# Kernel tuning notes

Hardware: AMD Instinct MI355X
Metric: run time of the kernel (lower is better)

Reference implementation:

```python
import jax, jax.numpy as jnp
import numpy as np

EMBED_DIM = 1024
N_HEADS = 16
HEAD_DIM = EMBED_DIM // N_HEADS
N_CATS = 5
SCALE = float(np.sqrt(HEAD_DIM))


def setup_inputs() -> dict:
    key = jax.random.key(0)
    ks = jax.random.split(key, 16)
    B, S = 2, 2048
    inp = {
        "query": jax.random.normal(ks[0], (B, S, EMBED_DIM), jnp.float32),
        "key_": jax.random.normal(ks[1], (B, S, EMBED_DIM), jnp.float32),
        "value": jax.random.normal(ks[2], (B, S, EMBED_DIM), jnp.float32),
        "responses": jax.random.randint(ks[3], (B, S), 0, N_CATS),
        "mask": jnp.ones((B, S, S), jnp.int32),
        # Linear params (torch convention: y = x @ W.T + b)
        "Wq": jax.random.normal(ks[4], (EMBED_DIM, EMBED_DIM), jnp.float32) * 0.02,
        "bq": jnp.zeros((EMBED_DIM,), jnp.float32),
        "Wk": jax.random.normal(ks[5], (EMBED_DIM, EMBED_DIM), jnp.float32) * 0.02,
        "bk": jnp.zeros((EMBED_DIM,), jnp.float32),
        "Wv": jax.random.normal(ks[6], (EMBED_DIM, EMBED_DIM), jnp.float32) * 0.02,
        "bv": jnp.zeros((EMBED_DIM,), jnp.float32),
        "Wo": jax.random.normal(ks[7], (EMBED_DIM, EMBED_DIM), jnp.float32) * 0.02,
        "bo": jnp.zeros((EMBED_DIM,), jnp.float32),
        # qwk_modulation: Linear(1, n_heads)
        "Wm": jax.random.normal(ks[8], (N_HEADS, 1), jnp.float32) * 0.5,
        "bm": jnp.zeros((N_HEADS,), jnp.float32),
    }
    return inp


def _qwk_matrix():
    i = jnp.arange(N_CATS, dtype=jnp.float32)
    return 1.0 - (i[:, None] - i[None, :]) ** 2 / (N_CATS - 1) ** 2  # [C, C]


def reference(query, key_, value, responses, mask,
              Wq, bq, Wk, bk, Wv, bv, Wo, bo, Wm, bm):
    B, S, E = query.shape
    # projections
    Q = (query @ Wq.T + bq).reshape(B, S, N_HEADS, HEAD_DIM).transpose(0, 2, 1, 3)
    K = (key_ @ Wk.T + bk).reshape(B, S, N_HEADS, HEAD_DIM).transpose(0, 2, 1, 3)
    V = (value @ Wv.T + bv).reshape(B, S, N_HEADS, HEAD_DIM).transpose(0, 2, 1, 3)
    scores = jnp.einsum("bhqd,bhkd->bhqk", Q, K) / SCALE  # [B,H,S,S]
    # QWK ordinal bias: gather pairwise weight, tiny linear 1->H, broadcast-add
    qwk = _qwk_matrix()
    pair = qwk[responses[:, :, None], responses[:, None, :]]  # [B,S,S]
    # Linear(1, n_heads): bias[...,None] @ Wm.T + bm -> [B,S,S,H] -> [B,H,S,S]
    head_bias = pair[:, None, :, :] * Wm[:, 0][None, :, None, None] + bm[None, :, None, None]
    scores = scores + head_bias
    scores = jnp.where(mask[:, None, :, :] == 0, -1e9, scores)
    attn = jax.nn.softmax(scores, axis=-1)
    attended = jnp.einsum("bhqk,bhkd->bhqd", attn, V)
    attended = attended.transpose(0, 2, 1, 3).reshape(B, S, E)
    return attended @ Wo.T + bo
```

## Files before the change

### kernel.cpp

```cpp
#include <hip/hip_runtime.h>
#include <hip/hip_bf16.h>
#include <stdint.h>

#define S_LEN 2048
#define EMB   1024
#define NHEAD 16
#define HDIM  64
#define BATCH 2

typedef __bf16 bf16x8 __attribute__((ext_vector_type(8)));
typedef float  f32x4  __attribute__((ext_vector_type(4)));

__device__ __forceinline__ void gll16(const void* g, void* l) {
  __builtin_amdgcn_global_load_lds(
      (const __attribute__((address_space(1))) void*)g,
      (__attribute__((address_space(3))) void*)l,
      16, 0, 0);
}

__global__ void __launch_bounds__(256) cast_mask_kernel(
    const float* __restrict__ s0, const float* __restrict__ s1, const float* __restrict__ s2,
    const float* __restrict__ s3, const float* __restrict__ s4, const float* __restrict__ s5,
    const float* __restrict__ s6,
    __hip_bfloat16* __restrict__ d0, __hip_bfloat16* __restrict__ d1,
    __hip_bfloat16* __restrict__ d2, __hip_bfloat16* __restrict__ d3,
    __hip_bfloat16* __restrict__ d4, __hip_bfloat16* __restrict__ d5,
    __hip_bfloat16* __restrict__ d6,
    const int* __restrict__ mask, unsigned* __restrict__ flags) {
  const int z = blockIdx.y;
  const int t = threadIdx.x;
  if (z == 7) {
    const int kt = blockIdx.x & 15, qt = (blockIdx.x >> 4) & 31, b = (int)blockIdx.x >> 9;
    const int* base = mask + ((size_t)b * S_LEN + (size_t)qt * 64) * S_LEN + (size_t)kt * 128;
    int ok = 1;
#pragma unroll
    for (int p = 0; p < 8; ++p) {
      int idx = p * 256 + t;
      int row = idx >> 5, c4 = idx & 31;
      const int4 v = *(const int4*)(base + (size_t)row * S_LEN + c4 * 4);
      ok &= (v.x != 0) & (v.y != 0) & (v.z != 0) & (v.w != 0);
    }
    unsigned long long bl = __ballot(ok);
    __shared__ unsigned long long bw[4];
    bw[t >> 6] = bl;
    __syncthreads();
    if (t == 0) {
      unsigned all = ((bw[0] & bw[1] & bw[2] & bw[3]) == ~0ull) ? 1u : 0u;
      flags[((size_t)b * 32 + qt) * 16 + kt] = all;
    }
    return;
  }
  const float* s = (z == 0) ? s0 : (z == 1) ? s1 : (z == 2) ? s2 : (z == 3) ? s3
                 : (z == 4) ? s4 : (z == 5) ? s5 : s6;
  __hip_bfloat16* d = (z == 0) ? d0 : (z == 1) ? d1 : (z == 2) ? d2 : (z == 3) ? d3
                    : (z == 4) ? d4 : (z == 5) ? d5 : d6;
  const int n = (z < 3) ? (BATCH * S_LEN * EMB) : (EMB * EMB);
  const size_t i = ((size_t)blockIdx.x * 256 + t) * 16;
  if (i >= (size_t)n) return;
  __hip_bfloat16 tmp[16];
#pragma unroll
  for (int j = 0; j < 4; ++j) {
    const float4 v = *(const float4*)(s + i + j * 4);
    tmp[j * 4 + 0] = __float2bfloat16(v.x);
    tmp[j * 4 + 1] = __float2bfloat16(v.y);
    tmp[j * 4 + 2] = __float2bfloat16(v.z);
    tmp[j * 4 + 3] = __float2bfloat16(v.w);
  }
  *(bf16x8*)(d + i)     = *(bf16x8*)&tmp[0];
  *(bf16x8*)(d + i + 8) = *(bf16x8*)&tmp[8];
}

__global__ void __launch_bounds__(256, 2)
gemm_kernel(const __hip_bfloat16* __restrict__ A0, const __hip_bfloat16* __restrict__ A1,
            const __hip_bfloat16* __restrict__ A2,
            const __hip_bfloat16* __restrict__ W0, const __hip_bfloat16* __restrict__ W1,
            const __hip_bfloat16* __restrict__ W2,
            const float* __restrict__ b0, const float* __restrict__ b1,
            const float* __restrict__ b2,
            __hip_bfloat16* __restrict__ O0, __hip_bfloat16* __restrict__ O1,
            __hip_bfloat16* __restrict__ O2) {
  __shared__ __align__(16) __hip_bfloat16 As[128 * 64];
  __shared__ __align__(16) __hip_bfloat16 Bs[128 * 64];

  const int L = blockIdx.x;
  const int m0 = (L & 31) * 128;
  const int n0 = ((L >> 5) & 7) * 128;
  const int z  = L >> 8;

  const __hip_bfloat16* A  = (z == 0) ? A0 : ((z == 1) ? A1 : A2);
  const __hip_bfloat16* W  = (z == 0) ? W0 : ((z == 1) ? W1 : W2);
  const float* bi          = (z == 0) ? b0 : ((z == 1) ? b1 : b2);
  __hip_bfloat16* O        = (z == 0) ? O0 : ((z == 1) ? O1 : O2);

  const int t = threadIdx.x;
  const int w = t >> 6, lane = t & 63, quad = lane >> 4, l15 = lane & 15;
  const int wr = w >> 1, wc = w & 1;

  f32x4 acc[4][4];
#pragma unroll
  for (int i = 0; i < 4; ++i)
#pragma unroll
    for (int j = 0; j < 4; ++j) acc[i][j] = (f32x4)0.0f;

  const int srow = t >> 3;
  const int scb  = (t & 7) ^ (srow & 7);
  const __hip_bfloat16* Ap = A + (size_t)(m0 + srow) * EMB + (scb << 3);
  const __hip_bfloat16* Wp = W + (size_t)(n0 + srow) * EMB + (scb << 3);

  for (int k0 = 0; k0 < EMB; k0 += 64) {
    __syncthreads();
#pragma unroll
    for (int rnd = 0; rnd < 4; ++rnd) {
      gll16(Ap + (size_t)(rnd * 32) * EMB + k0, &As[(rnd * 256 + (w << 6)) * 8]);
      gll16(Wp + (size_t)(rnd * 32) * EMB + k0, &Bs[(rnd * 256 + (w << 6)) * 8]);
    }
    __syncthreads();

    bf16x8 af[4][2], bfr[4][2];
#pragma unroll
    for (int i = 0; i < 4; ++i) {
      const int ra = wr * 64 + i * 16 + l15;
#pragma unroll
      for (int hh = 0; hh < 2; ++hh)
        af[i][hh] = *(const bf16x8*)&As[ra * 64 + ((((hh << 2) + quad) ^ (l15 & 7)) << 3)];
    }
#pragma unroll
    for (int j = 0; j < 4; ++j) {
      const int rbw = wc * 64 + j * 16 + l15;
#pragma unroll
      for (int hh = 0; hh < 2; ++hh)
        bfr[j][hh] = *(const bf16x8*)&Bs[rbw * 64 + ((((hh << 2) + quad) ^ (l15 & 7)) << 3)];
    }
#pragma unroll
    for (int hh = 0; hh < 2; ++hh)
#pragma unroll
      for (int i = 0; i < 4; ++i)
#pragma unroll
        for (int j = 0; j < 4; ++j)
          acc[i][j] =
              __builtin_amdgcn_mfma_f32_16x16x32_bf16(af[i][hh], bfr[j][hh], acc[i][j], 0, 0, 0);
  }

#pragma unroll
  for (int j = 0; j < 4; ++j) {
    const int ng = n0 + wc * 64 + j * 16 + l15;
    const float bb = bi[ng];
    const int h = ng >> 6, d = ng & 63;
#pragma unroll
    for (int i = 0; i < 4; ++i) {
#pragma unroll
      for (int r = 0; r < 4; ++r) {
        const int mg = m0 + wr * 64 + i * 16 + quad * 4 + r;
        const int b = mg >> 11, s = mg & 2047;
        float v = acc[i][j][r] + bb;
        if (z == 0) {
          O[(((size_t)b * NHEAD + h) * S_LEN + s) * HDIM + d] =
              __float2bfloat16(v * (0.125f * 1.4426950408889634f));
        } else if (z == 1) {
          O[(((size_t)b * NHEAD + h) * S_LEN + s) * HDIM + d] = __float2bfloat16(v);
        } else {
          const size_t idx = (size_t)(b * NHEAD + h) * 131072 + (size_t)(s >> 7) * 8192 +
                             (size_t)((((s >> 5) & 3) * 4 + ((s >> 2) & 3)) * 64 + d) * 8 +
                             ((s >> 4) & 1) * 4 + (s & 3);
          O[idx] = __float2bfloat16(v);
        }
      }
    }
  }
}

__global__ void __launch_bounds__(256, 2)
gemm_o_kernel(const __hip_bfloat16* __restrict__ A, const __hip_bfloat16* __restrict__ W,
              const float* __restrict__ bi, float* __restrict__ O) {
  __shared__ __align__(16) __hip_bfloat16 As[64 * 64];
  __shared__ __align__(16) __hip_bfloat16 Bs[128 * 64];
  const int L = blockIdx.x;
  const int m0 = (L & 63) * 64;
  const int n0 = (L >> 6) * 128;
  const int t = threadIdx.x;
  const int w = t >> 6, lane = t & 63, quad = lane >> 4, l15 = lane & 15;
  const int wr = w >> 1, wc = w & 1;

  f32x4 acc[2][4];
#pragma unroll
  for (int i = 0; i < 2; ++i)
#pragma unroll
    for (int j = 0; j < 4; ++j) acc[i][j] = (f32x4)0.0f;

  const int srow = t >> 3;
  const int scb  = (t & 7) ^ (srow & 7);
  const __hip_bfloat16* Ap = A + (size_t)(m0 + srow) * EMB + (scb << 3);
  const __hip_bfloat16* Wp = W + (size_t)(n0 + srow) * EMB + (scb << 3);

  for (int k0 = 0; k0 < EMB; k0 += 64) {
    __syncthreads();
#pragma unroll
    for (int rnd = 0; rnd < 2; ++rnd)
      gll16(Ap + (size_t)(rnd * 32) * EMB + k0, &As[(rnd * 256 + (w << 6)) * 8]);
#pragma unroll
    for (int rnd = 0; rnd < 4; ++rnd)
      gll16(Wp + (size_t)(rnd * 32) * EMB + k0, &Bs[(rnd * 256 + (w << 6)) * 8]);
    __syncthreads();

    bf16x8 af[2][2], bfr[4][2];
#pragma unroll
    for (int i = 0; i < 2; ++i) {
      const int ra = wr * 32 + i * 16 + l15;
#pragma unroll
      for (int hh = 0; hh < 2; ++hh)
        af[i][hh] = *(const bf16x8*)&As[ra * 64 + ((((hh << 2) + quad) ^ (l15 & 7)) << 3)];
    }
#pragma unroll
    for (int j = 0; j < 4; ++j) {
      const int rbw = wc * 64 + j * 16 + l15;
#pragma unroll
      for (int hh = 0; hh < 2; ++hh)
        bfr[j][hh] = *(const bf16x8*)&Bs[rbw * 64 + ((((hh << 2) + quad) ^ (l15 & 7)) << 3)];
    }
#pragma unroll
    for (int hh = 0; hh < 2; ++hh)
#pragma unroll
      for (int i = 0; i < 2; ++i)
#pragma unroll
        for (int j = 0; j < 4; ++j)
          acc[i][j] =
              __builtin_amdgcn_mfma_f32_16x16x32_bf16(af[i][hh], bfr[j][hh], acc[i][j], 0, 0, 0);
  }

#pragma unroll
  for (int j = 0; j < 4; ++j) {
    const int ng = n0 + wc * 64 + j * 16 + l15;
    const float bb = bi[ng];
#pragma unroll
    for (int i = 0; i < 2; ++i) {
#pragma unroll
      for (int r = 0; r < 4; ++r) {
        const int mg = m0 + wr * 32 + i * 16 + quad * 4 + r;
        O[(size_t)mg * EMB + ng] = acc[i][j][r] + bb;
      }
    }
  }
}

__global__ void __launch_bounds__(512, 4)
flash_kernel(const __hip_bfloat16* __restrict__ qws, const __hip_bfloat16* __restrict__ kws,
             const __hip_bfloat16* __restrict__ vpk, const int* __restrict__ responses,
             const int* __restrict__ mask, const float* __restrict__ Wm,
             const unsigned* __restrict__ flags, __hip_bfloat16* __restrict__ att) {
  __shared__ __align__(16) unsigned char smem[32768];
  __shared__ unsigned char rb[S_LEN];
  __shared__ float lsm[512];

  __hip_bfloat16* Ks = (__hip_bfloat16*)smem;
  __hip_bfloat16* Vs = (__hip_bfloat16*)(smem + 16384);
  float* sm = (float*)smem;

  const int t = threadIdx.x;
  const int w = t >> 6, lane = t & 63, quad = lane >> 4, l15 = lane & 15;
  const int L = blockIdx.x;
  const int bh = L & 31;
  const int qt = L >> 5;
  const int b = bh >> 4, h = bh & 15;
  const int q0 = qt * 128;
  const int wq = w & 3, khalf = w >> 2;

#pragma unroll
  for (int i = 0; i < 4; ++i)
    rb[i * 512 + t] = (unsigned char)responses[b * S_LEN + i * 512 + t];

  const __hip_bfloat16* qbase = qws + ((size_t)bh * S_LEN + q0 + wq * 32) * HDIM;
  bf16x8 qf[2][2];
#pragma unroll
  for (int qg = 0; qg < 2; ++qg)
#pragma unroll
    for (int ks = 0; ks < 2; ++ks)
      qf[qg][ks] =
          *(const bf16x8*)(qbase + (size_t)(qg * 16 + l15) * HDIM + ks * 32 + quad * 8);

  const float c = Wm[h] * (0.0625f * 1.4426950408889634f);
  float A2[2];
#pragma unroll
  for (int qg = 0; qg < 2; ++qg)
    A2[qg] = 2.0f * c * (float)responses[b * S_LEN + q0 + wq * 32 + qg * 16 + l15];

  const __hip_bfloat16* kptr = kws + ((size_t)bh * S_LEN + (t >> 3)) * HDIM +
                               (((t & 7) ^ ((t >> 3) & 7)) << 3);
  const __hip_bfloat16* vptr = vpk + (size_t)bh * 131072 + (size_t)t * 8;

  float lsum[2] = {0.f, 0.f};
  f32x4 acc_o[2][4];
#pragma unroll
  for (int qg = 0; qg < 2; ++qg)
#pragma unroll
    for (int dt = 0; dt < 4; ++dt) acc_o[qg][dt] = (f32x4)0.0f;

  for (int kt = 0; kt < S_LEN / 128; ++kt) {
    __syncthreads();
#pragma unroll
    for (int p = 0; p < 2; ++p) {
      gll16(kptr + p * 64 * HDIM, &Ks[(p * 512 + (w << 6)) * 8]);
      gll16(vptr + p * 4096,      &Vs[(p * 512 + (w << 6)) * 8]);
    }
    kptr += 128 * HDIM;
    vptr += 8192;
    __syncthreads();

    const unsigned fl = flags[((size_t)b * 32 + 2 * qt + (wq >> 1)) * 16 + kt];

    bf16x8 pfr[2][2];
#pragma unroll
    for (int ct = 0; ct < 4; ++ct) {
      const int rowk = khalf * 64 + ct * 16 + l15;
      bf16x8 kf0 = *(const bf16x8*)&Ks[rowk * 64 + ((quad ^ (l15 & 7)) << 3)];
      bf16x8 kf1 = *(const bf16x8*)&Ks[rowk * 64 + (((4 + quad) ^ (l15 & 7)) << 3)];
      const unsigned ru = *(const unsigned*)&rb[kt * 128 + khalf * 64 + ct * 16 + quad * 4];
#pragma unroll
      for (int qg = 0; qg < 2; ++qg) {
        f32x4 sc = __builtin_amdgcn_mfma_f32_16x16x32_bf16(kf0, qf[qg][0], (f32x4)0.0f, 0, 0, 0);
        sc = __builtin_amdgcn_mfma_f32_16x16x32_bf16(kf1, qf[qg][1], sc, 0, 0, 0);
        __hip_bfloat16 pb[4];
#pragma unroll
        for (int r = 0; r < 4; ++r) {
          const float rkf = (float)((ru >> (8 * r)) & 255u);
          const float sb = fmaf(rkf, fmaf(-c, rkf, A2[qg]), sc[r]);
          float p = __builtin_amdgcn_exp2f(sb);
          if (!fl) {
            int mq = mask[((size_t)b * S_LEN + q0 + wq * 32 + qg * 16 + l15) * S_LEN +
                          kt * 128 + khalf * 64 + ct * 16 + quad * 4 + r];
            p = mq ? p : 0.0f;
          }
          lsum[qg] += p;
          pb[r] = __float2bfloat16(p);
        }
        __hip_bfloat16* half = (__hip_bfloat16*)&pfr[qg][ct >> 1] + (ct & 1) * 4;
        half[0] = pb[0]; half[1] = pb[1]; half[2] = pb[2]; half[3] = pb[3];
      }
    }

#pragma unroll
    for (int ct2 = 0; ct2 < 2; ++ct2) {
      const int g2 = khalf * 2 + ct2;
#pragma unroll
      for (int dt = 0; dt < 4; ++dt) {
        bf16x8 vv = *(const bf16x8*)&Vs[(((g2 << 2) + quad) * 64 + (dt << 4) + l15) << 3];
#pragma unroll
        for (int qg = 0; qg < 2; ++qg)
          acc_o[qg][dt] =
              __builtin_amdgcn_mfma_f32_16x16x32_bf16(pfr[qg][ct2], vv, acc_o[qg][dt], 0, 0, 0);
      }
    }
  }

  __syncthreads();
  if (khalf == 0) {
#pragma unroll
    for (int qg = 0; qg < 2; ++qg) {
#pragma unroll
      for (int dt = 0; dt < 4; ++dt)
        *(f32x4*)&sm[((((wq << 1) + qg) << 2) + dt) * 256 + lane * 4] = acc_o[qg][dt];
      lsm[((wq << 1) + qg) * 64 + lane] = lsum[qg];
    }
  }
  __syncthreads();
  if (khalf == 1) {
#pragma unroll
    for (int qg = 0; qg < 2; ++qg) {
      lsum[qg] += lsm[((wq << 1) + qg) * 64 + lane];
      lsum[qg] += __shfl_xor(lsum[qg], 16, 64);
      lsum[qg] += __shfl_xor(lsum[qg], 32, 64);
#pragma unroll
      for (int dt = 0; dt < 4; ++dt)
        acc_o[qg][dt] += *(const f32x4*)&sm[((((wq << 1) + qg) << 2) + dt) * 256 + lane * 4];
      float inv[4];
#pragma unroll
      for (int r = 0; r < 4; ++r) inv[r] = 1.0f / __shfl(lsum[qg], quad * 4 + r, 64);
#pragma unroll
      for (int dt = 0; dt < 4; ++dt)
#pragma unroll
        for (int r = 0; r < 4; ++r)
          att[((size_t)b * S_LEN + q0 + wq * 32 + qg * 16 + quad * 4 + r) * EMB +
              h * HDIM + dt * 16 + l15] = __float2bfloat16(acc_o[qg][dt][r] * inv[r]);
    }
  }
}

extern "C" void kernel_launch(void* const* d_in, const int* in_sizes, int n_in,
                              void* d_out, int out_size, void* d_ws, size_t ws_size,
                              hipStream_t stream) {
  const float* query = (const float*)d_in[0];
  const float* key_  = (const float*)d_in[1];
  const float* value = (const float*)d_in[2];
  const int* responses = (const int*)d_in[3];
  const int* mask      = (const int*)d_in[4];
  const float* Wq = (const float*)d_in[5];
  const float* bq = (const float*)d_in[6];
  const float* Wk = (const float*)d_in[7];
  const float* bk = (const float*)d_in[8];
  const float* Wv = (const float*)d_in[9];
  const float* bv = (const float*)d_in[10];
  const float* Wo = (const float*)d_in[11];
  const float* bo = (const float*)d_in[12];
  const float* Wm = (const float*)d_in[13];

  __hip_bfloat16* ws = (__hip_bfloat16*)d_ws;
  const size_t NTOK = (size_t)BATCH * S_LEN * EMB;
  const size_t NW   = (size_t)EMB * EMB;
  __hip_bfloat16* qcast = ws;
  __hip_bfloat16* kcast = ws + NTOK;
  __hip_bfloat16* vcast = ws + 2 * NTOK;
  __hip_bfloat16* wqb   = ws + 3 * NTOK;
  __hip_bfloat16* wkb   = wqb + NW;
  __hip_bfloat16* wvb   = wqb + 2 * NW;
  __hip_bfloat16* wob   = wqb + 3 * NW;
  __hip_bfloat16* qws   = wqb + 4 * NW;
  __hip_bfloat16* kws   = qws + NTOK;
  __hip_bfloat16* vpk   = qws + 2 * NTOK;
  __hip_bfloat16* att   = qws + 3 * NTOK;
  unsigned* flags       = (unsigned*)(qws + 4 * NTOK);
  float* out            = (float*)d_out;

  cast_mask_kernel<<<dim3(1024, 8), 256, 0, stream>>>(
      query, key_, value, Wq, Wk, Wv, Wo,
      qcast, kcast, vcast, wqb, wkb, wvb, wob, mask, flags);
  gemm_kernel<<<768, 256, 0, stream>>>(qcast, kcast, vcast, wqb, wkb, wvb,
                                       bq, bk, bv, qws, kws, vpk);
  flash_kernel<<<512, 512, 0, stream>>>(qws, kws, vpk, responses, mask,
                                        Wm, flags, att);
  gemm_o_kernel<<<512, 256, 0, stream>>>(att, wob, bo, out);
}
```

Measured before the change: 249.0 us.

## Double-buffer K/V tiles in flash kernel and prefetch mask flags

Result: slower. 254.0 us (+2.0%).

```diff
diff --git a/kernel.cpp b/kernel.cpp
--- a/kernel.cpp
+++ b/kernel.cpp
@@ -247,12 +247,10 @@
              const __hip_bfloat16* __restrict__ vpk, const int* __restrict__ responses,
              const int* __restrict__ mask, const float* __restrict__ Wm,
              const unsigned* __restrict__ flags, __hip_bfloat16* __restrict__ att) {
-  __shared__ __align__(16) unsigned char smem[32768];
+  __shared__ __align__(16) unsigned char smem[65536];
   __shared__ unsigned char rb[S_LEN];
   __shared__ float lsm[512];
 
-  __hip_bfloat16* Ks = (__hip_bfloat16*)smem;
-  __hip_bfloat16* Vs = (__hip_bfloat16*)(smem + 16384);
   float* sm = (float*)smem;
 
   const int t = threadIdx.x;
@@ -283,6 +281,13 @@
   for (int qg = 0; qg < 2; ++qg)
     A2[qg] = 2.0f * c * (float)responses[b * S_LEN + q0 + wq * 32 + qg * 16 + l15];
 
+  unsigned fmask;
+  {
+    const unsigned fv =
+        flags[((size_t)b * 32 + 2 * qt + (wq >> 1)) * 16 + (lane & 15)];
+    fmask = (unsigned)__ballot(fv != 0u);
+  }
+
   const __hip_bfloat16* kptr = kws + ((size_t)bh * S_LEN + (t >> 3)) * HDIM +
                                (((t & 7) ^ ((t >> 3) & 7)) << 3);
   const __hip_bfloat16* vptr = vpk + (size_t)bh * 131072 + (size_t)t * 8;
@@ -294,18 +299,38 @@
 #pragma unroll
     for (int dt = 0; dt < 4; ++dt) acc_o[qg][dt] = (f32x4)0.0f;
 
-  for (int kt = 0; kt < S_LEN / 128; ++kt) {
-    __syncthreads();
+  {
+    __hip_bfloat16* Kd = (__hip_bfloat16*)smem;
+    __hip_bfloat16* Vd = Kd + 8192;
 #pragma unroll
     for (int p = 0; p < 2; ++p) {
-      gll16(kptr + p * 64 * HDIM, &Ks[(p * 512 + (w << 6)) * 8]);
-      gll16(vptr + p * 4096,      &Vs[(p * 512 + (w << 6)) * 8]);
+      gll16(kptr + p * 64 * HDIM, &Kd[(p * 512 + (w << 6)) * 8]);
+      gll16(vptr + p * 4096,      &Vd[(p * 512 + (w << 6)) * 8]);
     }
     kptr += 128 * HDIM;
     vptr += 8192;
-    __syncthreads();
-
-    const unsigned fl = flags[((size_t)b * 32 + 2 * qt + (wq >> 1)) * 16 + kt];
+  }
+  asm volatile("s_waitcnt vmcnt(0) lgkmcnt(0)" ::: "memory");
+  __builtin_amdgcn_s_barrier();
+  __builtin_amdgcn_sched_barrier(0);
+
+  int cur = 0;
+  for (int kt = 0; kt < S_LEN / 128; ++kt) {
+    if (kt < S_LEN / 128 - 1) {
+      __hip_bfloat16* Kd = (__hip_bfloat16*)(smem + (cur ? 0 : 32768));
+      __hip_bfloat16* Vd = Kd + 8192;
+#pragma unroll
+      for (int p = 0; p < 2; ++p) {
+        gll16(kptr + p * 64 * HDIM, &Kd[(p * 512 + (w << 6)) * 8]);
+        gll16(vptr + p * 4096,      &Vd[(p * 512 + (w << 6)) * 8]);
+      }
+      kptr += 128 * HDIM;
+      vptr += 8192;
+    }
+    const __hip_bfloat16* Ks = (const __hip_bfloat16*)(smem + (cur ? 32768 : 0));
+    const __hip_bfloat16* Vs = Ks + 8192;
+
+    const bool fl = (fmask >> kt) & 1u;
 
     bf16x8 pfr[2][2];
 #pragma unroll
@@ -316,8 +341,10 @@
       const unsigned ru = *(const unsigned*)&rb[kt * 128 + khalf * 64 + ct * 16 + quad * 4];
 #pragma unroll
       for (int qg = 0; qg < 2; ++qg) {
+        __builtin_amdgcn_s_setprio(1);
         f32x4 sc = __builtin_amdgcn_mfma_f32_16x16x32_bf16(kf0, qf[qg][0], (f32x4)0.0f, 0, 0, 0);
         sc = __builtin_amdgcn_mfma_f32_16x16x32_bf16(kf1, qf[qg][1], sc, 0, 0, 0);
+        __builtin_amdgcn_s_setprio(0);
         __hip_bfloat16 pb[4];
 #pragma unroll
         for (int r = 0; r < 4; ++r) {
@@ -343,15 +370,21 @@
 #pragma unroll
       for (int dt = 0; dt < 4; ++dt) {
         bf16x8 vv = *(const bf16x8*)&Vs[(((g2 << 2) + quad) * 64 + (dt << 4) + l15) << 3];
+        __builtin_amdgcn_s_setprio(1);
 #pragma unroll
         for (int qg = 0; qg < 2; ++qg)
           acc_o[qg][dt] =
               __builtin_amdgcn_mfma_f32_16x16x32_bf16(pfr[qg][ct2], vv, acc_o[qg][dt], 0, 0, 0);
+        __builtin_amdgcn_s_setprio(0);
       }
     }
-  }
-
-  __syncthreads();
+
+    asm volatile("s_waitcnt vmcnt(0)" ::: "memory");
+    __builtin_amdgcn_s_barrier();
+    __builtin_amdgcn_sched_barrier(0);
+    cur ^= 1;
+  }
+
   if (khalf == 0) {
 #pragma unroll
     for (int qg = 0; qg < 2; ++qg) {
```

## Halve flash query tile and split keys across four wave groups

Applied to the files above, without the earlier changes.

After: 498.0 us. 2x slower.

```diff
diff --git a/kernel.cpp b/kernel.cpp
--- a/kernel.cpp
+++ b/kernel.cpp
@@ -242,7 +242,7 @@
   }
 }
 
-__global__ void __launch_bounds__(512, 4)
+__global__ void __launch_bounds__(512, 8)
 flash_kernel(const __hip_bfloat16* __restrict__ qws, const __hip_bfloat16* __restrict__ kws,
              const __hip_bfloat16* __restrict__ vpk, const int* __restrict__ responses,
              const int* __restrict__ mask, const float* __restrict__ Wm,
@@ -261,8 +261,8 @@
   const int bh = L & 31;
   const int qt = L >> 5;
   const int b = bh >> 4, h = bh & 15;
-  const int q0 = qt * 128;
-  const int wq = w & 3, khalf = w >> 2;
+  const int q0 = qt * 64;
+  const int wq = w & 1, khalf = w >> 1;
 
 #pragma unroll
   for (int i = 0; i < 4; ++i)
@@ -283,6 +283,12 @@
   for (int qg = 0; qg < 2; ++qg)
     A2[qg] = 2.0f * c * (float)responses[b * S_LEN + q0 + wq * 32 + qg * 16 + l15];
 
+  unsigned fmask;
+  {
+    const unsigned fv = flags[((size_t)b * 32 + qt) * 16 + (lane & 15)];
+    fmask = (unsigned)__ballot(fv != 0u);
+  }
+
   const __hip_bfloat16* kptr = kws + ((size_t)bh * S_LEN + (t >> 3)) * HDIM +
                                (((t & 7) ^ ((t >> 3) & 7)) << 3);
   const __hip_bfloat16* vptr = vpk + (size_t)bh * 131072 + (size_t)t * 8;
@@ -305,15 +311,15 @@
     vptr += 8192;
     __syncthreads();
 
-    const unsigned fl = flags[((size_t)b * 32 + 2 * qt + (wq >> 1)) * 16 + kt];
-
-    bf16x8 pfr[2][2];
-#pragma unroll
-    for (int ct = 0; ct < 4; ++ct) {
-      const int rowk = khalf * 64 + ct * 16 + l15;
+    const bool fl = (fmask >> kt) & 1u;
+
+    bf16x8 pfr[2];
+#pragma unroll
+    for (int ct = 0; ct < 2; ++ct) {
+      const int rowk = khalf * 32 + ct * 16 + l15;
       bf16x8 kf0 = *(const bf16x8*)&Ks[rowk * 64 + ((quad ^ (l15 & 7)) << 3)];
       bf16x8 kf1 = *(const bf16x8*)&Ks[rowk * 64 + (((4 + quad) ^ (l15 & 7)) << 3)];
-      const unsigned ru = *(const unsigned*)&rb[kt * 128 + khalf * 64 + ct * 16 + quad * 4];
+      const unsigned ru = *(const unsigned*)&rb[kt * 128 + khalf * 32 + ct * 16 + quad * 4];
 #pragma unroll
       for (int qg = 0; qg < 2; ++qg) {
         f32x4 sc = __builtin_amdgcn_mfma_f32_16x16x32_bf16(kf0, qf[qg][0], (f32x4)0.0f, 0, 0, 0);
@@ -326,51 +332,70 @@
           float p = __builtin_amdgcn_exp2f(sb);
           if (!fl) {
             int mq = mask[((size_t)b * S_LEN + q0 + wq * 32 + qg * 16 + l15) * S_LEN +
-                          kt * 128 + khalf * 64 + ct * 16 + quad * 4 + r];
+                          kt * 128 + khalf * 32 + ct * 16 + quad * 4 + r];
             p = mq ? p : 0.0f;
           }
           lsum[qg] += p;
           pb[r] = __float2bfloat16(p);
         }
-        __hip_bfloat16* half = (__hip_bfloat16*)&pfr[qg][ct >> 1] + (ct & 1) * 4;
+        __hip_bfloat16* half = (__hip_bfloat16*)&pfr[qg] + ct * 4;
         half[0] = pb[0]; half[1] = pb[1]; half[2] = pb[2]; half[3] = pb[3];
       }
     }
 
 #pragma unroll
-    for (int ct2 = 0; ct2 < 2; ++ct2) {
-      const int g2 = khalf * 2 + ct2;
-#pragma unroll
-      for (int dt = 0; dt < 4; ++dt) {
-        bf16x8 vv = *(const bf16x8*)&Vs[(((g2 << 2) + quad) * 64 + (dt << 4) + l15) << 3];
-#pragma unroll
-        for (int qg = 0; qg < 2; ++qg)
-          acc_o[qg][dt] =
-              __builtin_amdgcn_mfma_f32_16x16x32_bf16(pfr[qg][ct2], vv, acc_o[qg][dt], 0, 0, 0);
-      }
-    }
-  }
-
+    for (int dt = 0; dt < 4; ++dt) {
+      bf16x8 vv = *(const bf16x8*)&Vs[(((khalf << 2) + quad) * 64 + (dt << 4) + l15) << 3];
+#pragma unroll
+      for (int qg = 0; qg < 2; ++qg)
+        acc_o[qg][dt] =
+            __builtin_amdgcn_mfma_f32_16x16x32_bf16(pfr[qg], vv, acc_o[qg][dt], 0, 0, 0);
+    }
+  }
+
+  __syncthreads();
+  if (khalf & 1) {
+    float* dst = sm + (khalf >> 1) * 4096;
+#pragma unroll
+    for (int qg = 0; qg < 2; ++qg) {
+#pragma unroll
+      for (int dt = 0; dt < 4; ++dt)
+        *(f32x4*)&dst[(((wq * 2 + qg) * 4) + dt) * 256 + lane * 4] = acc_o[qg][dt];
+      lsm[(khalf >> 1) * 256 + (wq * 2 + qg) * 64 + lane] = lsum[qg];
+    }
+  }
+  __syncthreads();
+  if (!(khalf & 1)) {
+    const float* src = sm + (khalf >> 1) * 4096;
+#pragma unroll
+    for (int qg = 0; qg < 2; ++qg) {
+#pragma unroll
+      for (int dt = 0; dt < 4; ++dt)
+        acc_o[qg][dt] += *(const f32x4*)&src[(((wq * 2 + qg) * 4) + dt) * 256 + lane * 4];
+      lsum[qg] += lsm[(khalf >> 1) * 256 + (wq * 2 + qg) * 64 + lane];
+    }
+  }
+  if (khalf == 2) {
+    float* dst = sm + 4096;
+#pragma unroll
+    for (int qg = 0; qg < 2; ++qg) {
+#pragma unroll
+      for (int dt = 0; dt < 4; ++dt)
+        *(f32x4*)&dst[(((wq * 2 + qg) * 4) + dt) * 256 + lane * 4] = acc_o[qg][dt];
+      lsm[256 + (wq * 2 + qg) * 64 + lane] = lsum[qg];
+    }
+  }
   __syncthreads();
   if (khalf == 0) {
+    const float* src = sm + 4096;
 #pragma unroll
     for (int qg = 0; qg < 2; ++qg) {
 #pragma unroll
       for (int dt = 0; dt < 4; ++dt)
-        *(f32x4*)&sm[((((wq << 1) + qg) << 2) + dt) * 256 + lane * 4] = acc_o[qg][dt];
-      lsm[((wq << 1) + qg) * 64 + lane] = lsum[qg];
-    }
-  }
-  __syncthreads();
-  if (khalf == 1) {
-#pragma unroll
-    for (int qg = 0; qg < 2; ++qg) {
-      lsum[qg] += lsm[((wq << 1) + qg) * 64 + lane];
+        acc_o[qg][dt] += *(const f32x4*)&src[(((wq * 2 + qg) * 4) + dt) * 256 + lane * 4];
+      lsum[qg] += lsm[256 + (wq * 2 + qg) * 64 + lane];
       lsum[qg] += __shfl_xor(lsum[qg], 16, 64);
       lsum[qg] += __shfl_xor(lsum[qg], 32, 64);
-#pragma unroll
-      for (int dt = 0; dt < 4; ++dt)
-        acc_o[qg][dt] += *(const f32x4*)&sm[((((wq << 1) + qg) << 2) + dt) * 256 + lane * 4];
       float inv[4];
 #pragma unroll
       for (int r = 0; r < 4; ++r) inv[r] = 1.0f / __shfl(lsum[qg], quad * 4 + r, 64);
@@ -424,7 +449,7 @@
       qcast, kcast, vcast, wqb, wkb, wvb, wob, mask, flags);
   gemm_kernel<<<768, 256, 0, stream>>>(qcast, kcast, vcast, wqb, wkb, wvb,
                                        bq, bk, bv, qws, kws, vpk);
-  flash_kernel<<<512, 512, 0, stream>>>(qws, kws, vpk, responses, mask,
-                                        Wm, flags, att);
+  flash_kernel<<<1024, 512, 0, stream>>>(qws, kws, vpk, responses, mask,
+                                         Wm, flags, att);
   gemm_o_kernel<<<512, 256, 0, stream>>>(att, wob, bo, out);
 }
```
